# Performance work log

Measured on AMD Instinct MI355X. Metric: run time of the kernel, lower is better.

Reference implementation:

```python
import jax, jax.numpy as jnp
import numpy as np

B, L = 1, 320
CS, CZ, CH, H, PQ, PV = 384, 128, 16, 12, 4, 8
INF, EPS = 1e5, 1e-8


def _quat_to_rot(q):
    w, x, y, z = q[..., 0], q[..., 1], q[..., 2], q[..., 3]
    r0 = jnp.stack([1 - 2*(y*y + z*z), 2*(x*y - w*z), 2*(x*z + w*y)], -1)
    r1 = jnp.stack([2*(x*y + w*z), 1 - 2*(x*x + z*z), 2*(y*z - w*x)], -1)
    r2 = jnp.stack([2*(x*z - w*y), 2*(y*z + w*x), 1 - 2*(x*x + y*y)], -1)
    return jnp.stack([r0, r1, r2], -2)


def setup_inputs():
    key = jax.random.key(0)
    ks = jax.random.split(key, 12)

    def lin(k, fan_in, fan_out):
        k1, k2 = jax.random.split(k)
        lim = 1.0 / np.sqrt(fan_in)
        return (jax.random.uniform(k1, (fan_in, fan_out), minval=-lim, maxval=lim, dtype=jnp.float32),
                jax.random.uniform(k2, (fan_out,), minval=-lim, maxval=lim, dtype=jnp.float32))

    s = jax.random.normal(ks[0], (B, L, CS), dtype=jnp.float32)
    quat = jax.random.normal(ks[1], (B, L, 4), dtype=jnp.float32)
    quat = quat / jnp.linalg.norm(quat, axis=-1, keepdims=True)
    rot = _quat_to_rot(quat)                                   # proper rotations (B,L,3,3)
    trans = 10.0 * jax.random.normal(ks[2], (B, L, 3), dtype=jnp.float32)
    z = jax.random.normal(ks[3], (B, L, L, CZ), dtype=jnp.float32)
    frame_mask = jnp.ones((B, L), dtype=jnp.float32)

    Wq, bq = lin(ks[4], CS, CH * H)
    Wkv, bkv = lin(ks[5], CS, 2 * CH * H)
    Wqp, bqp = lin(ks[6], CS, 6 * H * PQ)
    Wkvp, bkvp = lin(ks[7], CS, 6 * H * (PQ + PV))
    Wg, bg = lin(ks[8], CS, H * PQ)
    geom_weights = jnp.ones((3,), jnp.float32)
    dir_weight = jnp.asarray(0.5, jnp.float32)
    head_weights = 0.02 * jax.random.normal(ks[9], (H,), dtype=jnp.float32)
    concat_dim = H * (CH + 7 * PV) + H * CZ                    # 2400
    Wo, bo = lin(ks[10], concat_dim, CS)
    return dict(s=s, rot=rot, trans=trans, z=z, frame_mask=frame_mask,
                Wq=Wq, bq=bq, Wkv=Wkv, bkv=bkv, Wqp=Wqp, bqp=bqp,
                Wkvp=Wkvp, bkvp=bkvp, Wg=Wg, bg=bg,
                geom_weights=geom_weights, dir_weight=dir_weight,
                head_weights=head_weights, Wo=Wo, bo=bo)


def reference(s, rot, trans, z, frame_mask, Wq, bq, Wkv, bkv, Wqp, bqp,
              Wkvp, bkvp, Wg, bg, geom_weights, dir_weight, head_weights, Wo, bo):
    def proc_pts(pts_flat, P):
        # (B,L,6*H*P) -> rotate coords+translate, rotate dirs -> (B,L,H,P,6)
        pts = pts_flat.reshape(B, L, H, P, 6)
        coords = jnp.einsum('blij,blhpj->blhpi', rot, pts[..., :3]) + trans[:, :, None, None, :]
        dirs = jnp.einsum('blij,blhpj->blhpi', rot, pts[..., 3:])
        return jnp.concatenate([coords, dirs], -1)

    q = (s @ Wq + bq).reshape(B, L, H, CH)
    kv = s @ Wkv + bkv
    k = kv[..., :CH * H].reshape(B, L, H, CH)
    v = kv[..., CH * H:].reshape(B, L, H, CH)

    q_pts = proc_pts(s @ Wqp + bqp, PQ)
    kv_pts = s @ Wkvp + bkvp
    k_pts = proc_pts(kv_pts[..., :6 * H * PQ], PQ)
    v_pts = proc_pts(kv_pts[..., 6 * H * PQ:], PV)

    gate = jax.nn.sigmoid(s @ Wg + bg).reshape(B, L, H, PQ, 1)
    q_pts = q_pts * gate

    scalar_att = jnp.einsum('bqhc,bkhc->bhqk', q, k) / np.sqrt(CH).astype(np.float32)

    # position attention: per-pair point distances + log + inverse, mean over points
    delta = q_pts[:, :, None, :, :, :3] - k_pts[:, None, :, :, :, :3]   # (B,Lq,Lk,H,PQ,3)
    d = jnp.linalg.norm(delta, axis=-1)
    pos_att = (d + jnp.log(d + EPS) + 1.0 / (d + EPS)).mean(-1).transpose(0, 3, 1, 2)

    # direction attention: per-point dot minus cross-product 'curvature'
    qd, kd = q_pts[..., 3:], k_pts[..., 3:]
    dot = jnp.einsum('bqhpd,bkhpd->bqkhp', qd, kd)                       # (B,Lq,Lk,H,P)
    cr = jnp.cross(qd[:, :, None, :, None, :, :], kd[:, None, :, :, :, None, :])  # (B,Lq,Lk,H,Pk,Pq,3)
    cross = jnp.linalg.norm(cr, axis=-1).mean(-1)                        # (B,Lq,Lk,H,Pk)
    nq = jnp.linalg.norm(qd, axis=-1)[:, :, None]                        # (B,Lq,1,H,P)
    nk = jnp.linalg.norm(kd, axis=-1)[:, None]                           # (B,1,Lk,H,P)
    dir_att = (dot - cross / (nq * nk + EPS)).mean(-1).transpose(0, 3, 1, 2)

    att = scalar_att + dir_weight * (geom_weights[0] * pos_att + geom_weights[1] * dir_att)
    att = att * head_weights[:, None, None]
    mask2d = frame_mask[:, None, None, :] * frame_mask[:, None, :, None]  # (B,1,L,L)
    att = jax.nn.softmax(att + INF * (mask2d - 1.0), axis=-1)

    o_scalar = jnp.einsum('bhqk,bkhc->bqhc', att, v)
    o_geom = jnp.einsum('bhqk,bkhpd->bqhpd', att, v_pts)                 # (B,L,H,PV,6)

    # map aggregated geometry back into local frames
    rotT = jnp.swapaxes(rot, -1, -2)
    trans_inv = -jnp.einsum('blij,blj->bli', rotT, trans)
    lc = jnp.einsum('blij,blhpj->blhpi', rotT, o_geom[..., :3]) + trans_inv[:, :, None, None, :]
    ld = jnp.einsum('blij,blhpj->blhpi', rotT, o_geom[..., 3:6])
    ld = ld / jnp.maximum(jnp.linalg.norm(ld, axis=-1, keepdims=True), 1e-12)  # F.normalize
    ln = jnp.linalg.norm(lc, axis=-1, keepdims=True)
    o_geom7 = jnp.concatenate([lc, ld, ln], -1)                          # (B,L,H,PV,7)

    o_pair = jnp.einsum('bhij,bijk->bihk', att, z)                       # (B,L,H,CZ)
    out = jnp.concatenate([o_scalar.reshape(B, L, H * CH),
                           o_geom7.reshape(B, L, H * PV * 7),
                           o_pair.reshape(B, L, H * CZ)], -1)
    return out @ Wo + bo
```

## Files before the change

### kernel.cpp

```cpp
#include <hip/hip_runtime.h>
#include <hip/hip_bf16.h>
#include <math.h>

#define LSEQ 320
#define CS 384
#define CZ 128
#define CH 16
#define NH 12
#define PQ 4
#define PV 8
#define EPSF 1e-8f

typedef short short8 __attribute__((ext_vector_type(8)));
typedef float f32x4 __attribute__((ext_vector_type(4)));
typedef unsigned short ush2 __attribute__((ext_vector_type(2)));

__device__ __forceinline__ unsigned short f2b(float x) {
    union { float f; unsigned u; } v; v.f = x;
    unsigned r = (v.u + 0x7FFF + ((v.u >> 16) & 1)) >> 16;
    return (unsigned short)r;
}
__device__ __forceinline__ float b2f(unsigned short h) {
    union { unsigned u; float f; } v; v.u = ((unsigned)h) << 16;
    return v.f;
}

#define OFF_Q       0
#define OFF_KV      61440
#define OFF_QPT     184320
#define OFF_SHI     276480
#define OFF_SMID    337920
#define OFF_SLO     399360
#define OFF_ATTHI   552960
#define OFF_PARTG   552960
#define OFF_CCHI    2191360
#define OFF_BCAT    4074496
#define OFF_VKVHI   4997872
#define OFF_VKVLO   5120752
#define OFF_QPR     5243632
#define OFF_KVPR    5335792
#define OFF_GATE    5612272
#define OFF_KROW    6242032
#define OFF_WCTHI   6426352
#define OFF_WCTMID  6767344
#define OFF_WCTLO   7108336
#define OFF_WOTHI   7449328
#define OFF_WOTLO   7910128

__global__ __launch_bounds__(256) void k_cast(
    const float* __restrict__ s,
    const float* __restrict__ bq, const float* __restrict__ bkv,
    const float* __restrict__ bqp, const float* __restrict__ bkvp,
    const float* __restrict__ bg,
    unsigned short* __restrict__ s_hi, unsigned short* __restrict__ s_mid,
    unsigned short* __restrict__ s_lo,
    float* __restrict__ bcat)
{
    int i = blockIdx.x * 256 + threadIdx.x;
    if (i < 122880) {
        float x = s[i];
        unsigned short hi = f2b(x);
        float r1 = x - b2f(hi);
        unsigned short mid = f2b(r1);
        s_hi[i] = hi; s_mid[i] = mid; s_lo[i] = f2b(r1 - b2f(mid));
        return;
    }
    i -= 122880;
    if (i < 1776) {
        float v;
        if (i < 192)       v = bq[i];
        else if (i < 576)  v = bkv[i - 192];
        else if (i < 864)  v = bqp[i - 576];
        else if (i < 1728) v = bkvp[i - 864];
        else               v = bg[i - 1728];
        bcat[i] = v;
    }
}

__global__ __launch_bounds__(256) void k_wtr(
    const float* __restrict__ Wq, const float* __restrict__ Wkv,
    const float* __restrict__ Wqp, const float* __restrict__ Wkvp,
    const float* __restrict__ Wg, const float* __restrict__ Wo,
    unsigned short* __restrict__ wcT_hi, unsigned short* __restrict__ wcT_mid,
    unsigned short* __restrict__ wcT_lo,
    unsigned short* __restrict__ woT_hi, unsigned short* __restrict__ woT_lo)
{
    __shared__ unsigned short th[64][65], tm[64][65], tl[64][65];
    int bid = blockIdx.x, tid = threadIdx.x;
    if (bid < 168) {
        int k0 = (bid % 6) * 64, c0 = (bid / 6) * 64;
        #pragma unroll
        for (int rep = 0; rep < 16; rep++) {
            int idx = rep * 256 + tid;
            int i = idx >> 6, j = idx & 63;
            int c = c0 + j, k = k0 + i;
            float v = 0.f;
            if (c < 1776) {
                if (c < 192)       v = Wq[(size_t)k * 192 + c];
                else if (c < 576)  v = Wkv[(size_t)k * 384 + c - 192];
                else if (c < 864)  v = Wqp[(size_t)k * 288 + c - 576];
                else if (c < 1728) v = Wkvp[(size_t)k * 864 + c - 864];
                else               v = Wg[(size_t)k * 48 + c - 1728];
            }
            unsigned short hi = f2b(v);
            float r1 = v - b2f(hi);
            unsigned short mid = f2b(r1);
            th[i][j] = hi; tm[i][j] = mid; tl[i][j] = f2b(r1 - b2f(mid));
        }
        __syncthreads();
        #pragma unroll
        for (int rep = 0; rep < 16; rep++) {
            int idx = rep * 256 + tid;
            int i = idx >> 6, j = idx & 63;
            int c = c0 + i;
            if (c < 1776) {
                size_t o = (size_t)c * 384 + k0 + j;
                wcT_hi[o] = th[j][i]; wcT_mid[o] = tm[j][i]; wcT_lo[o] = tl[j][i];
            }
        }
    } else {
        int b = bid - 168;
        int r0 = (b % 38) * 64, c0 = (b / 38) * 64;
        #pragma unroll
        for (int rep = 0; rep < 16; rep++) {
            int idx = rep * 256 + tid;
            int i = idx >> 6, j = idx & 63;
            int r = r0 + i;
            float v = 0.f;
            if (r < 2400) v = Wo[(size_t)r * 384 + c0 + j];
            unsigned short hi = f2b(v);
            th[i][j] = hi; tl[i][j] = f2b(v - b2f(hi));
        }
        __syncthreads();
        #pragma unroll
        for (int rep = 0; rep < 16; rep++) {
            int idx = rep * 256 + tid;
            int i = idx >> 6, j = idx & 63;
            int r = r0 + j;
            if (r < 2400) {
                size_t o = (size_t)(c0 + i) * 2400 + r;
                woT_hi[o] = th[j][i]; woT_lo[o] = tl[j][i];
            }
        }
    }
}

__global__ __launch_bounds__(192) void k_proj(
    const unsigned short* __restrict__ s_hi, const unsigned short* __restrict__ s_mid,
    const unsigned short* __restrict__ s_lo,
    const unsigned short* __restrict__ wcT_hi, const unsigned short* __restrict__ wcT_mid,
    const unsigned short* __restrict__ wcT_lo,
    const float* __restrict__ bcat,
    float* __restrict__ qo, float* __restrict__ kvo,
    float* __restrict__ qpr, float* __restrict__ kvpr, float* __restrict__ gate)
{
    __shared__ unsigned short a_h[16][56], a_m[16][56], a_l[16][56];
    __shared__ unsigned short w_h[48][56], w_m[48][56], w_l[48][56];
    int col0 = blockIdx.x * 48, l0 = blockIdx.y * 16;
    int tid = threadIdx.x;
    int lane = tid & 63, w = tid >> 6;
    int ncol = lane & 15, blk = lane >> 4, mrow = (lane >> 4) * 4;

    float* dst; int nc, cbase; bool sig = false;
    if (col0 < 192)       { nc = 192; cbase = col0;        dst = qo;   }
    else if (col0 < 576)  { nc = 384; cbase = col0 - 192;  dst = kvo;  }
    else if (col0 < 864)  { nc = 288; cbase = col0 - 576;  dst = qpr;  }
    else if (col0 < 1728) { nc = 864; cbase = col0 - 864;  dst = kvpr; }
    else                  { nc = 48;  cbase = 0;           dst = gate; sig = true; }

    f32x4 acc = {};
    for (int k0 = 0; k0 < 384; k0 += 32) {
        __syncthreads();
        {
            int arr = tid >> 6, idx = tid & 63;
            int row = idx >> 2, seg = idx & 3;
            size_t off = (size_t)(l0 + row) * 384 + k0 + seg * 8;
            if (arr == 0)      *(short8*)&a_h[row][seg * 8] = *(const short8*)(s_hi + off);
            else if (arr == 1) *(short8*)&a_m[row][seg * 8] = *(const short8*)(s_mid + off);
            else               *(short8*)&a_l[row][seg * 8] = *(const short8*)(s_lo + off);
        }
        {
            int row = tid >> 2, seg = tid & 3;
            size_t off = (size_t)(col0 + row) * 384 + k0 + seg * 8;
            *(short8*)&w_h[row][seg * 8] = *(const short8*)(wcT_hi + off);
            *(short8*)&w_m[row][seg * 8] = *(const short8*)(wcT_mid + off);
            *(short8*)&w_l[row][seg * 8] = *(const short8*)(wcT_lo + off);
        }
        __syncthreads();
        short8 afh = *(short8*)&a_h[ncol][blk * 8];
        short8 afm = *(short8*)&a_m[ncol][blk * 8];
        short8 afl = *(short8*)&a_l[ncol][blk * 8];
        short8 bfh = *(short8*)&w_h[w * 16 + ncol][blk * 8];
        short8 bfm = *(short8*)&w_m[w * 16 + ncol][blk * 8];
        short8 bfl = *(short8*)&w_l[w * 16 + ncol][blk * 8];
        acc = __builtin_amdgcn_mfma_f32_16x16x32_bf16(afm, bfm, acc, 0, 0, 0);
        acc = __builtin_amdgcn_mfma_f32_16x16x32_bf16(afh, bfl, acc, 0, 0, 0);
        acc = __builtin_amdgcn_mfma_f32_16x16x32_bf16(afl, bfh, acc, 0, 0, 0);
        acc = __builtin_amdgcn_mfma_f32_16x16x32_bf16(afh, bfm, acc, 0, 0, 0);
        acc = __builtin_amdgcn_mfma_f32_16x16x32_bf16(afm, bfh, acc, 0, 0, 0);
        acc = __builtin_amdgcn_mfma_f32_16x16x32_bf16(afh, bfh, acc, 0, 0, 0);
    }
    {
        int n = w * 16 + ncol;
        float bv = bcat[col0 + n];
        int cloc = cbase + n;
        #pragma unroll
        for (int r = 0; r < 4; r++) {
            float v2 = acc[r] + bv;
            if (sig) v2 = 1.0f / (1.0f + expf(-v2));
            dst[(size_t)(l0 + mrow + r) * nc + cloc] = v2;
        }
    }
}

__global__ __launch_bounds__(256) void k_points(
    const float* __restrict__ qpr, const float* __restrict__ kvpr, const float* __restrict__ gate,
    const float* __restrict__ rot, const float* __restrict__ trans,
    const float* __restrict__ kv,
    float* __restrict__ qpt, float* __restrict__ krow,
    unsigned short* __restrict__ vkv_hi, unsigned short* __restrict__ vkv_lo)
{
    __shared__ float vsh[96][6];
    __shared__ float kp_s[48][6];
    __shared__ float kn_s[48];
    int l = blockIdx.x, t = threadIdx.x;
    const float* R = rot + l * 9;
    float tx = trans[l * 3], ty = trans[l * 3 + 1], tz = trans[l * 3 + 2];
    if (t < 192) {
        const float* src; float g = 1.0f; float* dst = nullptr; int vj = -1, kj = -1;
        if (t < 48)      { src = qpr + (size_t)l * 288 + t * 6; g = gate[l * 48 + t]; dst = qpt + ((size_t)l * 48 + t) * 6; }
        else if (t < 96) { kj = t - 48; src = kvpr + (size_t)l * 864 + kj * 6; }
        else             { int j = t - 96; src = kvpr + (size_t)l * 864 + 288 + j * 6; vj = j; }
        float px = src[0], py = src[1], pz = src[2], ux = src[3], uy = src[4], uz = src[5];
        float c0 = R[0] * px + R[1] * py + R[2] * pz + tx;
        float c1 = R[3] * px + R[4] * py + R[5] * pz + ty;
        float c2 = R[6] * px + R[7] * py + R[8] * pz + tz;
        float d0 = R[0] * ux + R[1] * uy + R[2] * uz;
        float d1 = R[3] * ux + R[4] * uy + R[5] * uz;
        float d2 = R[6] * ux + R[7] * uy + R[8] * uz;
        if (vj >= 0) {
            vsh[vj][0] = c0; vsh[vj][1] = c1; vsh[vj][2] = c2;
            vsh[vj][3] = d0; vsh[vj][4] = d1; vsh[vj][5] = d2;
        } else if (kj >= 0) {
            kp_s[kj][0] = c0; kp_s[kj][1] = c1; kp_s[kj][2] = c2;
            kp_s[kj][3] = d0; kp_s[kj][4] = d1; kp_s[kj][5] = d2;
            kn_s[kj] = sqrtf(d0 * d0 + d1 * d1 + d2 * d2);
        } else {
            dst[0] = c0 * g; dst[1] = c1 * g; dst[2] = c2 * g;
            dst[3] = d0 * g; dst[4] = d1 * g; dst[5] = d2 * g;
        }
    }
    __syncthreads();
    #pragma unroll
    for (int e = 0; e < 3; e++) {
        int u = t * 3 + e;
        int h = u >> 6, n = u & 63;
        float val;
        if (n < 16) val = kv[(size_t)l * 384 + 192 + h * 16 + n];
        else        val = vsh[h * 8 + (n - 16) / 6][(n - 16) % 6];
        unsigned short hi = f2b(val);
        size_t idx = ((size_t)h * 64 + n) * 320 + l;
        vkv_hi[idx] = hi;
        vkv_lo[idx] = f2b(val - b2f(hi));
    }
    for (int idx = t; idx < 576; idx += 256) {
        int h = idx / 48, j = idx - h * 48;
        float v;
        if (j < 24)      v = kp_s[h * 4 + j / 6][j % 6];
        else if (j < 40) v = kv[(size_t)l * 384 + h * 16 + (j - 24)];
        else if (j < 44) v = kn_s[h * 4 + (j - 40)];
        else             v = 0.0f;
        krow[((size_t)h * 320 + l) * 48 + j] = v;
    }
}

__global__ __launch_bounds__(256) void k_att(
    const float* __restrict__ qb, const float* __restrict__ qpt,
    const float* __restrict__ krow,
    const float* __restrict__ fm, const float* __restrict__ gw,
    const float* __restrict__ dwp, const float* __restrict__ hwp,
    float* __restrict__ att)
{
    int tid = threadIdx.x;
    int w = tid >> 6, lane = tid & 63;
    int iqA = blockIdx.x * 8 + w * 2;
    int iqB = iqA + 1;
    int h = blockIdx.y;

    float qvA[CH], qvB[CH];
    #pragma unroll
    for (int c = 0; c < CH; c++) {
        qvA[c] = qb[(size_t)iqA * 192 + h * CH + c];
        qvB[c] = qb[(size_t)iqB * 192 + h * CH + c];
    }
    float qpA[24], qpB[24];
    #pragma unroll
    for (int j = 0; j < 24; j++) {
        qpA[j] = qpt[(size_t)iqA * 288 + h * 24 + j];
        qpB[j] = qpt[(size_t)iqB * 288 + h * 24 + j];
    }
    float nqA[PQ], nq2A[PQ], nqB[PQ], nq2B[PQ];
    #pragma unroll
    for (int p = 0; p < PQ; p++) {
        float x = qpA[p * 6 + 3], y = qpA[p * 6 + 4], zz = qpA[p * 6 + 5];
        nq2A[p] = x * x + y * y + zz * zz; nqA[p] = sqrtf(nq2A[p]);
        x = qpB[p * 6 + 3]; y = qpB[p * 6 + 4]; zz = qpB[p * 6 + 5];
        nq2B[p] = x * x + y * y + zz * zz; nqB[p] = sqrtf(nq2B[p]);
    }
    float dwv = dwp[0], g0 = gw[0], g1 = gw[1], hwv = hwp[h];
    float fmA = fm[iqA], fmB = fm[iqB];

    float lgA[5], lgB[5];
    for (int r = 0; r < 5; r++) {
        int kk = r * 64 + lane;
        const float* rowp = krow + ((size_t)h * 320 + kk) * 48;
        float rw[44];
        #pragma unroll
        for (int j = 0; j < 44; j++) rw[j] = rowp[j];
        float fmk = fm[kk];

        #pragma unroll
        for (int which = 0; which < 2; which++) {
            const float* qp = which ? qpB : qpA;
            const float* qv = which ? qvB : qvA;
            const float* nq = which ? nqB : nqA;
            const float* nq2 = which ? nq2B : nq2A;
            float fmi = which ? fmB : fmA;

            float scalar = 0.f;
            #pragma unroll
            for (int c = 0; c < CH; c++) scalar += qv[c] * rw[24 + c];
            scalar *= 0.25f;

            float pos = 0.f;
            #pragma unroll
            for (int p = 0; p < PQ; p++) {
                float dx = qp[p * 6] - rw[p * 6];
                float dy = qp[p * 6 + 1] - rw[p * 6 + 1];
                float dz = qp[p * 6 + 2] - rw[p * 6 + 2];
                float d = __builtin_amdgcn_sqrtf(dx * dx + dy * dy + dz * dz);
                float de = d + EPSF;
                pos += d + __logf(de) + __builtin_amdgcn_rcpf(de);
            }
            pos *= 0.25f;

            float dir = 0.f;
            #pragma unroll
            for (int p = 0; p < PQ; p++) {
                float kx = rw[p * 6 + 3], ky = rw[p * 6 + 4], kz = rw[p * 6 + 5];
                float nk = rw[40 + p];
                float nk2 = nk * nk;
                float cm = 0.f, dself = 0.f;
                #pragma unroll
                for (int pq = 0; pq < PQ; pq++) {
                    float dq = qp[pq * 6 + 3] * kx + qp[pq * 6 + 4] * ky + qp[pq * 6 + 5] * kz;
                    if (pq == p) dself = dq;
                    cm += __builtin_amdgcn_sqrtf(fmaxf(nq2[pq] * nk2 - dq * dq, 0.0f));
                }
                cm *= 0.25f;
                dir += dself - cm * __builtin_amdgcn_rcpf(nq[p] * nk + EPSF);
            }
            dir *= 0.25f;

            float logit = scalar + dwv * (g0 * pos + g1 * dir);
            logit *= hwv;
            logit += 100000.0f * (fmi * fmk - 1.0f);
            if (which) lgB[r] = logit; else lgA[r] = logit;
        }
    }

    float mxA = lgA[0];
    #pragma unroll
    for (int r = 1; r < 5; r++) mxA = fmaxf(mxA, lgA[r]);
    for (int m = 32; m; m >>= 1) mxA = fmaxf(mxA, __shfl_xor(mxA, m, 64));
    float eA[5], smA = 0.f;
    #pragma unroll
    for (int r = 0; r < 5; r++) { eA[r] = __expf(lgA[r] - mxA); smA += eA[r]; }
    for (int m = 32; m; m >>= 1) smA += __shfl_xor(smA, m, 64);
    float invA = 1.0f / smA;
    #pragma unroll
    for (int r = 0; r < 5; r++)
        att[((size_t)h * 320 + iqA) * 320 + r * 64 + lane] = eA[r] * invA;
    float mxB = lgB[0];
    #pragma unroll
    for (int r = 1; r < 5; r++) mxB = fmaxf(mxB, lgB[r]);
    for (int m = 32; m; m >>= 1) mxB = fmaxf(mxB, __shfl_xor(mxB, m, 64));
    float eB[5], smB = 0.f;
    #pragma unroll
    for (int r = 0; r < 5; r++) { eB[r] = __expf(lgB[r] - mxB); smB += eB[r]; }
    for (int m = 32; m; m >>= 1) smB += __shfl_xor(smB, m, 64);
    float invB = 1.0f / smB;
    #pragma unroll
    for (int r = 0; r < 5; r++)
        att[((size_t)h * 320 + iqB) * 320 + r * 64 + lane] = eB[r] * invB;
}

__global__ __launch_bounds__(256) void k_sv(
    const float* __restrict__ att,
    const unsigned short* __restrict__ vkv_hi, const unsigned short* __restrict__ vkv_lo,
    const float* __restrict__ rot, const float* __restrict__ trans,
    float* __restrict__ cc)
{
    __shared__ unsigned short a_hi[16][56];
    __shared__ unsigned short a_lo[16][56];
    __shared__ unsigned short B[128][56];
    __shared__ float ogsh[16][49];
    int bid = blockIdx.x;
    int iq0 = (bid % 20) * 16, h = bid / 20;
    int tid = threadIdx.x;
    int lane = tid & 63, w = tid >> 6;
    int ncol = lane & 15, blk = lane >> 4, mrow = (lane >> 4) * 4;

    f32x4 acc = {};
    for (int k0 = 0; k0 < 320; k0 += 32) {
        __syncthreads();
        {
            int row = tid >> 4, c2 = (tid & 15) * 2;
            const float* ap = att + ((size_t)h * 320 + iq0 + row) * 320 + k0 + c2;
            float v0 = ap[0], v1 = ap[1];
            ush2 h2, l2;
            h2[0] = f2b(v0); l2[0] = f2b(v0 - b2f(h2[0]));
            h2[1] = f2b(v1); l2[1] = f2b(v1 - b2f(h2[1]));
            *(ush2*)&a_hi[row][c2] = h2;
            *(ush2*)&a_lo[row][c2] = l2;
        }
        {
            int row = tid >> 2, seg = tid & 3;
            size_t off = ((size_t)h * 64 + row) * 320 + k0 + seg * 8;
            *(short8*)&B[row][seg * 8]      = *(const short8*)(vkv_hi + off);
            *(short8*)&B[64 + row][seg * 8] = *(const short8*)(vkv_lo + off);
        }
        __syncthreads();
        short8 afh = *(short8*)&a_hi[ncol][blk * 8];
        short8 afl = *(short8*)&a_lo[ncol][blk * 8];
        short8 bfh = *(short8*)&B[w * 16 + ncol][blk * 8];
        short8 bfl = *(short8*)&B[64 + w * 16 + ncol][blk * 8];
        acc = __builtin_amdgcn_mfma_f32_16x16x32_bf16(afh, bfh, acc, 0, 0, 0);
        acc = __builtin_amdgcn_mfma_f32_16x16x32_bf16(afh, bfl, acc, 0, 0, 0);
        acc = __builtin_amdgcn_mfma_f32_16x16x32_bf16(afl, bfh, acc, 0, 0, 0);
    }
    {
        int n = w * 16 + ncol;
        #pragma unroll
        for (int r = 0; r < 4; r++) {
            int iq = iq0 + mrow + r;
            float v = acc[r];
            if (n < 16) cc[(size_t)iq * 2400 + h * 16 + n] = v;
            else        ogsh[mrow + r][n - 16] = v;
        }
    }
    __syncthreads();
    if (tid < 128) {
        int iqr = tid >> 3, p = tid & 7;
        int l = iq0 + iqr;
        const float* R = rot + l * 9;
        float tx = trans[l * 3], ty = trans[l * 3 + 1], tz = trans[l * 3 + 2];
        const float* o = &ogsh[iqr][p * 6];
        float gx = o[0] - tx, gy = o[1] - ty, gz = o[2] - tz;
        float l0 = R[0] * gx + R[3] * gy + R[6] * gz;
        float l1 = R[1] * gx + R[4] * gy + R[7] * gz;
        float l2 = R[2] * gx + R[5] * gy + R[8] * gz;
        float dx = o[3], dy = o[4], dz = o[5];
        float e0 = R[0] * dx + R[3] * dy + R[6] * dz;
        float e1 = R[1] * dx + R[4] * dy + R[7] * dz;
        float e2 = R[2] * dx + R[5] * dy + R[8] * dz;
        float n = sqrtf(e0 * e0 + e1 * e1 + e2 * e2);
        float inv = 1.0f / fmaxf(n, 1e-12f);
        float ln = sqrtf(l0 * l0 + l1 * l1 + l2 * l2);
        float vals[7] = { l0, l1, l2, e0 * inv, e1 * inv, e2 * inv, ln };
        size_t base = (size_t)l * 2400 + 192 + (h * PV + p) * 7;
        #pragma unroll
        for (int j = 0; j < 7; j++) cc[base + j] = vals[j];
    }
}

__global__ __launch_bounds__(256) void k_pair(
    const float* __restrict__ att,
    const float* __restrict__ z,
    float* __restrict__ cc)
{
    __shared__ unsigned short a_hi[16][56];
    __shared__ unsigned short a_lo[16][56];
    __shared__ unsigned short B[128][56];
    int iq = blockIdx.x, tid = threadIdx.x;
    int lane = tid & 63, w = tid >> 6;
    int ncol = lane & 15, blk = lane >> 4, mrow = (lane >> 4) * 4;
    int kp2 = (tid & 15) * 2;
    int cb = (tid >> 4) * 8;
    const float* zbase = z + ((size_t)iq * 320 + kp2) * 128 + cb;

    float4 zA0, zA1, zA2, zA3, zB0, zB1, zB2, zB3;
    {
        const float* p = zbase;
        zA0 = *(const float4*)(p);       zA1 = *(const float4*)(p + 4);
        zA2 = *(const float4*)(p + 128); zA3 = *(const float4*)(p + 132);
        p = zbase + (size_t)32 * 128;
        zB0 = *(const float4*)(p);       zB1 = *(const float4*)(p + 4);
        zB2 = *(const float4*)(p + 128); zB3 = *(const float4*)(p + 132);
    }

    f32x4 acc[2] = {};
    #pragma unroll
    for (int i = 0; i < 10; i++) {
        int k0 = i * 32;
        __syncthreads();
        {
            int row = tid >> 4, c2 = (tid & 15) * 2;
            float v0 = 0.f, v1 = 0.f;
            if (row < 12) {
                const float* ap = att + ((size_t)row * 320 + iq) * 320 + k0 + c2;
                v0 = ap[0]; v1 = ap[1];
            }
            ush2 h2, l2;
            h2[0] = f2b(v0); l2[0] = f2b(v0 - b2f(h2[0]));
            h2[1] = f2b(v1); l2[1] = f2b(v1 - b2f(h2[1]));
            *(ush2*)&a_hi[row][c2] = h2;
            *(ush2*)&a_lo[row][c2] = l2;
        }
        {
            float va[8], vb[8];
            if ((i & 1) == 0) {
                va[0]=zA0.x; va[1]=zA0.y; va[2]=zA0.z; va[3]=zA0.w;
                va[4]=zA1.x; va[5]=zA1.y; va[6]=zA1.z; va[7]=zA1.w;
                vb[0]=zA2.x; vb[1]=zA2.y; vb[2]=zA2.z; vb[3]=zA2.w;
                vb[4]=zA3.x; vb[5]=zA3.y; vb[6]=zA3.z; vb[7]=zA3.w;
            } else {
                va[0]=zB0.x; va[1]=zB0.y; va[2]=zB0.z; va[3]=zB0.w;
                va[4]=zB1.x; va[5]=zB1.y; va[6]=zB1.z; va[7]=zB1.w;
                vb[0]=zB2.x; vb[1]=zB2.y; vb[2]=zB2.z; vb[3]=zB2.w;
                vb[4]=zB3.x; vb[5]=zB3.y; vb[6]=zB3.z; vb[7]=zB3.w;
            }
            #pragma unroll
            for (int c = 0; c < 8; c++) {
                ush2 pr;
                pr[0] = f2b(va[c]);
                pr[1] = f2b(vb[c]);
                *(ush2*)&B[cb + c][kp2] = pr;
            }
            if (i + 2 < 10) {
                const float* p = zbase + (size_t)(k0 + 64) * 128;
                if ((i & 1) == 0) {
                    zA0 = *(const float4*)(p);       zA1 = *(const float4*)(p + 4);
                    zA2 = *(const float4*)(p + 128); zA3 = *(const float4*)(p + 132);
                } else {
                    zB0 = *(const float4*)(p);       zB1 = *(const float4*)(p + 4);
                    zB2 = *(const float4*)(p + 128); zB3 = *(const float4*)(p + 132);
                }
            }
        }
        __syncthreads();
        short8 afh = *(short8*)&a_hi[ncol][blk * 8];
        short8 afl = *(short8*)&a_lo[ncol][blk * 8];
        #pragma unroll
        for (int s2 = 0; s2 < 2; s2++) {
            short8 bf = *(short8*)&B[w * 32 + s2 * 16 + ncol][blk * 8];
            acc[s2] = __builtin_amdgcn_mfma_f32_16x16x32_bf16(afl, bf, acc[s2], 0, 0, 0);
            acc[s2] = __builtin_amdgcn_mfma_f32_16x16x32_bf16(afh, bf, acc[s2], 0, 0, 0);
        }
    }
    #pragma unroll
    for (int s2 = 0; s2 < 2; s2++) {
        int n = w * 32 + s2 * 16 + ncol;
        #pragma unroll
        for (int r = 0; r < 4; r++) {
            int h = mrow + r;
            if (h < 12)
                cc[(size_t)iq * 2400 + 864 + (size_t)h * 128 + n] = acc[s2][r];
        }
    }
}

__global__ __launch_bounds__(256) void k_gemm(
    const float* __restrict__ cc,
    const unsigned short* __restrict__ woT_hi, const unsigned short* __restrict__ woT_lo,
    float* __restrict__ part)
{
    __shared__ unsigned short a_h[16][56], a_l[16][56];
    __shared__ unsigned short w_h[64][56], w_l[64][56];
    int iq0 = blockIdx.x * 16, col0 = blockIdx.y * 64, ks = blockIdx.z;
    int tid = threadIdx.x;
    int lane = tid & 63, w = tid >> 6;
    int ncol = lane & 15, blk = lane >> 4, mrow = (lane >> 4) * 4;

    f32x4 acc = {};
    for (int kc = 0; kc < 15; kc++) {
        int k0 = ks * 480 + kc * 32;
        __syncthreads();
        {
            int row = tid >> 4, c2 = (tid & 15) * 2;
            const float* ap = cc + (size_t)(iq0 + row) * 2400 + k0 + c2;
            float v0 = ap[0], v1 = ap[1];
            ush2 h2, l2;
            h2[0] = f2b(v0); l2[0] = f2b(v0 - b2f(h2[0]));
            h2[1] = f2b(v1); l2[1] = f2b(v1 - b2f(h2[1]));
            *(ush2*)&a_h[row][c2] = h2;
            *(ush2*)&a_l[row][c2] = l2;
        }
        #pragma unroll
        for (int t2 = 0; t2 < 2; t2++) {
            int idx = tid * 2 + t2;
            int arr = idx >> 8, i2 = idx & 255;
            int row = i2 >> 2, seg = i2 & 3;
            size_t off = (size_t)(col0 + row) * 2400 + k0 + seg * 8;
            if (arr == 0) *(short8*)&w_h[row][seg * 8] = *(const short8*)(woT_hi + off);
            else          *(short8*)&w_l[row][seg * 8] = *(const short8*)(woT_lo + off);
        }
        __syncthreads();
        short8 afh = *(short8*)&a_h[ncol][blk * 8];
        short8 afl = *(short8*)&a_l[ncol][blk * 8];
        short8 bfh = *(short8*)&w_h[w * 16 + ncol][blk * 8];
        short8 bfl = *(short8*)&w_l[w * 16 + ncol][blk * 8];
        acc = __builtin_amdgcn_mfma_f32_16x16x32_bf16(afh, bfh, acc, 0, 0, 0);
        acc = __builtin_amdgcn_mfma_f32_16x16x32_bf16(afh, bfl, acc, 0, 0, 0);
        acc = __builtin_amdgcn_mfma_f32_16x16x32_bf16(afl, bfh, acc, 0, 0, 0);
    }
    {
        int cn = col0 + w * 16 + ncol;
        #pragma unroll
        for (int r = 0; r < 4; r++)
            part[((size_t)ks * 320 + iq0 + mrow + r) * 384 + cn] = acc[r];
    }
}

__global__ __launch_bounds__(256) void k_reduce(
    const float* __restrict__ part, const float* __restrict__ bo, float* __restrict__ out)
{
    int i = blockIdx.x * 256 + threadIdx.x;
    float v = bo[i % CS];
    #pragma unroll
    for (int ks = 0; ks < 5; ks++) v += part[(size_t)ks * 122880 + i];
    out[i] = v;
}

extern "C" void kernel_launch(void* const* d_in, const int* in_sizes, int n_in,
                              void* d_out, int out_size, void* d_ws, size_t ws_size,
                              hipStream_t stream)
{
    const float* s     = (const float*)d_in[0];
    const float* rot   = (const float*)d_in[1];
    const float* trans = (const float*)d_in[2];
    const float* z     = (const float*)d_in[3];
    const float* fm    = (const float*)d_in[4];
    const float* Wq    = (const float*)d_in[5];
    const float* bq    = (const float*)d_in[6];
    const float* Wkv   = (const float*)d_in[7];
    const float* bkv   = (const float*)d_in[8];
    const float* Wqp   = (const float*)d_in[9];
    const float* bqp   = (const float*)d_in[10];
    const float* Wkvp  = (const float*)d_in[11];
    const float* bkvp  = (const float*)d_in[12];
    const float* Wg    = (const float*)d_in[13];
    const float* bg    = (const float*)d_in[14];
    const float* gw    = (const float*)d_in[15];
    const float* dw    = (const float*)d_in[16];
    const float* hw    = (const float*)d_in[17];
    const float* Wo    = (const float*)d_in[18];
    const float* bo    = (const float*)d_in[19];

    float* ws = (float*)d_ws;
    float*          q       = ws + OFF_Q;
    float*          kv      = ws + OFF_KV;
    float*          qpt     = ws + OFF_QPT;
    float*          att     = ws + OFF_ATTHI;
    float*          part    = ws + OFF_PARTG;
    float*          cc      = ws + OFF_CCHI;
    unsigned short* s_hi    = (unsigned short*)(ws + OFF_SHI);
    unsigned short* s_mid   = (unsigned short*)(ws + OFF_SMID);
    unsigned short* s_lo    = (unsigned short*)(ws + OFF_SLO);
    float*          bcat    = ws + OFF_BCAT;
    unsigned short* vkv_hi  = (unsigned short*)(ws + OFF_VKVHI);
    unsigned short* vkv_lo  = (unsigned short*)(ws + OFF_VKVLO);
    float*          qpr     = ws + OFF_QPR;
    float*          kvpr    = ws + OFF_KVPR;
    float*          gate    = ws + OFF_GATE;
    float*          krow    = ws + OFF_KROW;
    unsigned short* wcT_hi  = (unsigned short*)(ws + OFF_WCTHI);
    unsigned short* wcT_mid = (unsigned short*)(ws + OFF_WCTMID);
    unsigned short* wcT_lo  = (unsigned short*)(ws + OFF_WCTLO);
    unsigned short* woT_hi  = (unsigned short*)(ws + OFF_WOTHI);
    unsigned short* woT_lo  = (unsigned short*)(ws + OFF_WOTLO);
    float* out = (float*)d_out;

    k_cast<<<dim3(487), dim3(256), 0, stream>>>(s, bq, bkv, bqp, bkvp, bg,
                                                s_hi, s_mid, s_lo, bcat);
    k_wtr<<<dim3(396), dim3(256), 0, stream>>>(Wq, Wkv, Wqp, Wkvp, Wg, Wo,
                                               wcT_hi, wcT_mid, wcT_lo, woT_hi, woT_lo);
    k_proj<<<dim3(37, 20), dim3(192), 0, stream>>>(s_hi, s_mid, s_lo, wcT_hi, wcT_mid, wcT_lo,
                                                   bcat, q, kv, qpr, kvpr, gate);
    k_points<<<dim3(LSEQ), dim3(256), 0, stream>>>(qpr, kvpr, gate, rot, trans, kv,
                                                   qpt, krow, vkv_hi, vkv_lo);
    k_att<<<dim3(40, NH), dim3(256), 0, stream>>>(q, qpt, krow, fm, gw, dw, hw, att);
    k_sv<<<dim3(240), dim3(256), 0, stream>>>(att, vkv_hi, vkv_lo, rot, trans, cc);
    k_pair<<<dim3(LSEQ), dim3(256), 0, stream>>>(att, z, cc);
    k_gemm<<<dim3(20, 6, 5), dim3(256), 0, stream>>>(cc, woT_hi, woT_lo, part);
    k_reduce<<<dim3(480), dim3(256), 0, stream>>>(part, bo, out);
}
```

Measured before the change: 213.0 us.

## Merge prep kernels and sv/pair kernels; stage key rows in LDS for attention

Merges the cast and weight-transpose kernels into one launch, and the scalar/point value aggregation and pair aggregation kernels into one launch with block-index dispatch. This cuts launch count and lets independent blocks fill the GPU together. The attention kernel now loads the per-head key rows (320x45 floats) into shared memory once per block instead of reading them from global memory in each wave. The large shared array may reduce occupancy in k_att.

```diff
diff --git a/kernel.cpp b/kernel.cpp
--- a/kernel.cpp
+++ b/kernel.cpp
@@ -47,46 +47,45 @@
 #define OFF_WOTHI   7449328
 #define OFF_WOTLO   7910128
 
-__global__ __launch_bounds__(256) void k_cast(
+__global__ __launch_bounds__(256) void k_prep(
     const float* __restrict__ s,
-    const float* __restrict__ bq, const float* __restrict__ bkv,
-    const float* __restrict__ bqp, const float* __restrict__ bkvp,
-    const float* __restrict__ bg,
+    const float* __restrict__ Wq, const float* __restrict__ bq,
+    const float* __restrict__ Wkv, const float* __restrict__ bkv,
+    const float* __restrict__ Wqp, const float* __restrict__ bqp,
+    const float* __restrict__ Wkvp, const float* __restrict__ bkvp,
+    const float* __restrict__ Wg, const float* __restrict__ bg,
+    const float* __restrict__ Wo,
     unsigned short* __restrict__ s_hi, unsigned short* __restrict__ s_mid,
-    unsigned short* __restrict__ s_lo,
-    float* __restrict__ bcat)
-{
-    int i = blockIdx.x * 256 + threadIdx.x;
-    if (i < 122880) {
-        float x = s[i];
-        unsigned short hi = f2b(x);
-        float r1 = x - b2f(hi);
-        unsigned short mid = f2b(r1);
-        s_hi[i] = hi; s_mid[i] = mid; s_lo[i] = f2b(r1 - b2f(mid));
-        return;
-    }
-    i -= 122880;
-    if (i < 1776) {
-        float v;
-        if (i < 192)       v = bq[i];
-        else if (i < 576)  v = bkv[i - 192];
-        else if (i < 864)  v = bqp[i - 576];
-        else if (i < 1728) v = bkvp[i - 864];
-        else               v = bg[i - 1728];
-        bcat[i] = v;
-    }
-}
-
-__global__ __launch_bounds__(256) void k_wtr(
-    const float* __restrict__ Wq, const float* __restrict__ Wkv,
-    const float* __restrict__ Wqp, const float* __restrict__ Wkvp,
-    const float* __restrict__ Wg, const float* __restrict__ Wo,
+    unsigned short* __restrict__ s_lo, float* __restrict__ bcat,
     unsigned short* __restrict__ wcT_hi, unsigned short* __restrict__ wcT_mid,
     unsigned short* __restrict__ wcT_lo,
     unsigned short* __restrict__ woT_hi, unsigned short* __restrict__ woT_lo)
 {
     __shared__ unsigned short th[64][65], tm[64][65], tl[64][65];
     int bid = blockIdx.x, tid = threadIdx.x;
+    if (bid < 487) {
+        int i = bid * 256 + tid;
+        if (i < 122880) {
+            float x = s[i];
+            unsigned short hi = f2b(x);
+            float r1 = x - b2f(hi);
+            unsigned short mid = f2b(r1);
+            s_hi[i] = hi; s_mid[i] = mid; s_lo[i] = f2b(r1 - b2f(mid));
+            return;
+        }
+        i -= 122880;
+        if (i < 1776) {
+            float v;
+            if (i < 192)       v = bq[i];
+            else if (i < 576)  v = bkv[i - 192];
+            else if (i < 864)  v = bqp[i - 576];
+            else if (i < 1728) v = bkvp[i - 864];
+            else               v = bg[i - 1728];
+            bcat[i] = v;
+        }
+        return;
+    }
+    bid -= 487;
     if (bid < 168) {
         int k0 = (bid % 6) * 64, c0 = (bid / 6) * 64;
         #pragma unroll
@@ -281,12 +280,18 @@
     const float* __restrict__ dwp, const float* __restrict__ hwp,
     float* __restrict__ att)
 {
+    __shared__ float ksh[320][45];
     int tid = threadIdx.x;
     int w = tid >> 6, lane = tid & 63;
     int iqA = blockIdx.x * 8 + w * 2;
     int iqB = iqA + 1;
     int h = blockIdx.y;
 
+    for (int idx = tid; idx < 320 * 48; idx += 256) {
+        int kk = idx / 48, j = idx - kk * 48;
+        if (j < 45) ksh[kk][j] = krow[((size_t)h * 320 + kk) * 48 + j];
+    }
+
     float qvA[CH], qvB[CH];
     #pragma unroll
     for (int c = 0; c < CH; c++) {
@@ -309,11 +314,12 @@
     }
     float dwv = dwp[0], g0 = gw[0], g1 = gw[1], hwv = hwp[h];
     float fmA = fm[iqA], fmB = fm[iqB];
+    __syncthreads();
 
     float lgA[5], lgB[5];
     for (int r = 0; r < 5; r++) {
         int kk = r * 64 + lane;
-        const float* rowp = krow + ((size_t)h * 320 + kk) * 48;
+        const float* rowp = &ksh[kk][0];
         float rw[44];
         #pragma unroll
         for (int j = 0; j < 44; j++) rw[j] = rowp[j];
@@ -395,9 +401,10 @@
         att[((size_t)h * 320 + iqB) * 320 + r * 64 + lane] = eB[r] * invB;
 }
 
-__global__ __launch_bounds__(256) void k_sv(
+__global__ __launch_bounds__(256) void k_svpair(
     const float* __restrict__ att,
     const unsigned short* __restrict__ vkv_hi, const unsigned short* __restrict__ vkv_lo,
+    const float* __restrict__ z,
     const float* __restrict__ rot, const float* __restrict__ trans,
     float* __restrict__ cc)
 {
@@ -406,166 +413,157 @@
     __shared__ unsigned short B[128][56];
     __shared__ float ogsh[16][49];
     int bid = blockIdx.x;
-    int iq0 = (bid % 20) * 16, h = bid / 20;
     int tid = threadIdx.x;
     int lane = tid & 63, w = tid >> 6;
     int ncol = lane & 15, blk = lane >> 4, mrow = (lane >> 4) * 4;
 
-    f32x4 acc = {};
-    for (int k0 = 0; k0 < 320; k0 += 32) {
+    if (bid < 240) {
+        int iq0 = (bid % 20) * 16, h = bid / 20;
+        f32x4 acc = {};
+        for (int k0 = 0; k0 < 320; k0 += 32) {
+            __syncthreads();
+            {
+                int row = tid >> 4, c2 = (tid & 15) * 2;
+                const float* ap = att + ((size_t)h * 320 + iq0 + row) * 320 + k0 + c2;
+                float v0 = ap[0], v1 = ap[1];
+                ush2 h2, l2;
+                h2[0] = f2b(v0); l2[0] = f2b(v0 - b2f(h2[0]));
+                h2[1] = f2b(v1); l2[1] = f2b(v1 - b2f(h2[1]));
+                *(ush2*)&a_hi[row][c2] = h2;
+                *(ush2*)&a_lo[row][c2] = l2;
+            }
+            {
+                int row = tid >> 2, seg = tid & 3;
+                size_t off = ((size_t)h * 64 + row) * 320 + k0 + seg * 8;
+                *(short8*)&B[row][seg * 8]      = *(const short8*)(vkv_hi + off);
+                *(short8*)&B[64 + row][seg * 8] = *(const short8*)(vkv_lo + off);
+            }
+            __syncthreads();
+            short8 afh = *(short8*)&a_hi[ncol][blk * 8];
+            short8 afl = *(short8*)&a_lo[ncol][blk * 8];
+            short8 bfh = *(short8*)&B[w * 16 + ncol][blk * 8];
+            short8 bfl = *(short8*)&B[64 + w * 16 + ncol][blk * 8];
+            acc = __builtin_amdgcn_mfma_f32_16x16x32_bf16(afh, bfh, acc, 0, 0, 0);
+            acc = __builtin_amdgcn_mfma_f32_16x16x32_bf16(afh, bfl, acc, 0, 0, 0);
+            acc = __builtin_amdgcn_mfma_f32_16x16x32_bf16(afl, bfh, acc, 0, 0, 0);
+        }
+        {
+            int n = w * 16 + ncol;
+            #pragma unroll
+            for (int r = 0; r < 4; r++) {
+                int iq = iq0 + mrow + r;
+                float v = acc[r];
+                if (n < 16) cc[(size_t)iq * 2400 + h * 16 + n] = v;
+                else        ogsh[mrow + r][n - 16] = v;
+            }
+        }
         __syncthreads();
+        if (tid < 128) {
+            int iqr = tid >> 3, p = tid & 7;
+            int l = iq0 + iqr;
+            const float* R = rot + l * 9;
+            float tx = trans[l * 3], ty = trans[l * 3 + 1], tz = trans[l * 3 + 2];
+            const float* o = &ogsh[iqr][p * 6];
+            float gx = o[0] - tx, gy = o[1] - ty, gz = o[2] - tz;
+            float l0 = R[0] * gx + R[3] * gy + R[6] * gz;
+            float l1 = R[1] * gx + R[4] * gy + R[7] * gz;
+            float l2 = R[2] * gx + R[5] * gy + R[8] * gz;
+            float dx = o[3], dy = o[4], dz = o[5];
+            float e0 = R[0] * dx + R[3] * dy + R[6] * dz;
+            float e1 = R[1] * dx + R[4] * dy + R[7] * dz;
+            float e2 = R[2] * dx + R[5] * dy + R[8] * dz;
+            float n = sqrtf(e0 * e0 + e1 * e1 + e2 * e2);
+            float inv = 1.0f / fmaxf(n, 1e-12f);
+            float ln = sqrtf(l0 * l0 + l1 * l1 + l2 * l2);
+            float vals[7] = { l0, l1, l2, e0 * inv, e1 * inv, e2 * inv, ln };
+            size_t base = (size_t)l * 2400 + 192 + (h * PV + p) * 7;
+            #pragma unroll
+            for (int j = 0; j < 7; j++) cc[base + j] = vals[j];
+        }
+    } else {
+        int iq = bid - 240;
+        int kp2 = (tid & 15) * 2;
+        int cb = (tid >> 4) * 8;
+        const float* zbase = z + ((size_t)iq * 320 + kp2) * 128 + cb;
+
+        float4 zA0, zA1, zA2, zA3, zB0, zB1, zB2, zB3;
         {
-            int row = tid >> 4, c2 = (tid & 15) * 2;
-            const float* ap = att + ((size_t)h * 320 + iq0 + row) * 320 + k0 + c2;
-            float v0 = ap[0], v1 = ap[1];
-            ush2 h2, l2;
-            h2[0] = f2b(v0); l2[0] = f2b(v0 - b2f(h2[0]));
-            h2[1] = f2b(v1); l2[1] = f2b(v1 - b2f(h2[1]));
-            *(ush2*)&a_hi[row][c2] = h2;
-            *(ush2*)&a_lo[row][c2] = l2;
-        }
-        {
-            int row = tid >> 2, seg = tid & 3;
-            size_t off = ((size_t)h * 64 + row) * 320 + k0 + seg * 8;
-            *(short8*)&B[row][seg * 8]      = *(const short8*)(vkv_hi + off);
-            *(short8*)&B[64 + row][seg * 8] = *(const short8*)(vkv_lo + off);
-        }
-        __syncthreads();
-        short8 afh = *(short8*)&a_hi[ncol][blk * 8];
-        short8 afl = *(short8*)&a_lo[ncol][blk * 8];
-        short8 bfh = *(short8*)&B[w * 16 + ncol][blk * 8];
-        short8 bfl = *(short8*)&B[64 + w * 16 + ncol][blk * 8];
-        acc = __builtin_amdgcn_mfma_f32_16x16x32_bf16(afh, bfh, acc, 0, 0, 0);
-        acc = __builtin_amdgcn_mfma_f32_16x16x32_bf16(afh, bfl, acc, 0, 0, 0);
-        acc = __builtin_amdgcn_mfma_f32_16x16x32_bf16(afl, bfh, acc, 0, 0, 0);
-    }
-    {
-        int n = w * 16 + ncol;
-        #pragma unroll
-        for (int r = 0; r < 4; r++) {
-            int iq = iq0 + mrow + r;
-            float v = acc[r];
-            if (n < 16) cc[(size_t)iq * 2400 + h * 16 + n] = v;
-            else        ogsh[mrow + r][n - 16] = v;
-        }
-    }
-    __syncthreads();
-    if (tid < 128) {
-        int iqr = tid >> 3, p = tid & 7;
-        int l = iq0 + iqr;
-        const float* R = rot + l * 9;
-        float tx = trans[l * 3], ty = trans[l * 3 + 1], tz = trans[l * 3 + 2];
-        const float* o = &ogsh[iqr][p * 6];
-        float gx = o[0] - tx, gy = o[1] - ty, gz = o[2] - tz;
-        float l0 = R[0] * gx + R[3] * gy + R[6] * gz;
-        float l1 = R[1] * gx + R[4] * gy + R[7] * gz;
-        float l2 = R[2] * gx + R[5] * gy + R[8] * gz;
-        float dx = o[3], dy = o[4], dz = o[5];
-        float e0 = R[0] * dx + R[3] * dy + R[6] * dz;
-        float e1 = R[1] * dx + R[4] * dy + R[7] * dz;
-        float e2 = R[2] * dx + R[5] * dy + R[8] * dz;
-        float n = sqrtf(e0 * e0 + e1 * e1 + e2 * e2);
-        float inv = 1.0f / fmaxf(n, 1e-12f);
-        float ln = sqrtf(l0 * l0 + l1 * l1 + l2 * l2);
-        float vals[7] = { l0, l1, l2, e0 * inv, e1 * inv, e2 * inv, ln };
-        size_t base = (size_t)l * 2400 + 192 + (h * PV + p) * 7;
-        #pragma unroll
-        for (int j = 0; j < 7; j++) cc[base + j] = vals[j];
-    }
-}
-
-__global__ __launch_bounds__(256) void k_pair(
-    const float* __restrict__ att,
-    const float* __restrict__ z,
-    float* __restrict__ cc)
-{
-    __shared__ unsigned short a_hi[16][56];
-    __shared__ unsigned short a_lo[16][56];
-    __shared__ unsigned short B[128][56];
-    int iq = blockIdx.x, tid = threadIdx.x;
-    int lane = tid & 63, w = tid >> 6;
-    int ncol = lane & 15, blk = lane >> 4, mrow = (lane >> 4) * 4;
-    int kp2 = (tid & 15) * 2;
-    int cb = (tid >> 4) * 8;
-    const float* zbase = z + ((size_t)iq * 320 + kp2) * 128 + cb;
-
-    float4 zA0, zA1, zA2, zA3, zB0, zB1, zB2, zB3;
-    {
-        const float* p = zbase;
-        zA0 = *(const float4*)(p);       zA1 = *(const float4*)(p + 4);
-        zA2 = *(const float4*)(p + 128); zA3 = *(const float4*)(p + 132);
-        p = zbase + (size_t)32 * 128;
-        zB0 = *(const float4*)(p);       zB1 = *(const float4*)(p + 4);
-        zB2 = *(const float4*)(p + 128); zB3 = *(const float4*)(p + 132);
-    }
-
-    f32x4 acc[2] = {};
-    #pragma unroll
-    for (int i = 0; i < 10; i++) {
-        int k0 = i * 32;
-        __syncthreads();
-        {
-            int row = tid >> 4, c2 = (tid & 15) * 2;
-            float v0 = 0.f, v1 = 0.f;
-            if (row < 12) {
-                const float* ap = att + ((size_t)row * 320 + iq) * 320 + k0 + c2;
-                v0 = ap[0]; v1 = ap[1];
-            }
-            ush2 h2, l2;
-            h2[0] = f2b(v0); l2[0] = f2b(v0 - b2f(h2[0]));
-            h2[1] = f2b(v1); l2[1] = f2b(v1 - b2f(h2[1]));
-            *(ush2*)&a_hi[row][c2] = h2;
-            *(ush2*)&a_lo[row][c2] = l2;
-        }
-        {
-            float va[8], vb[8];
-            if ((i & 1) == 0) {
-                va[0]=zA0.x; va[1]=zA0.y; va[2]=zA0.z; va[3]=zA0.w;
-                va[4]=zA1.x; va[5]=zA1.y; va[6]=zA1.z; va[7]=zA1.w;
-                vb[0]=zA2.x; vb[1]=zA2.y; vb[2]=zA2.z; vb[3]=zA2.w;
-                vb[4]=zA3.x; vb[5]=zA3.y; vb[6]=zA3.z; vb[7]=zA3.w;
-            } else {
-                va[0]=zB0.x; va[1]=zB0.y; va[2]=zB0.z; va[3]=zB0.w;
-                va[4]=zB1.x; va[5]=zB1.y; va[6]=zB1.z; va[7]=zB1.w;
-                vb[0]=zB2.x; vb[1]=zB2.y; vb[2]=zB2.z; vb[3]=zB2.w;
-                vb[4]=zB3.x; vb[5]=zB3.y; vb[6]=zB3.z; vb[7]=zB3.w;
-            }
+            const float* p = zbase;
+            zA0 = *(const float4*)(p);       zA1 = *(const float4*)(p + 4);
+            zA2 = *(const float4*)(p + 128); zA3 = *(const float4*)(p + 132);
+            p = zbase + (size_t)32 * 128;
+            zB0 = *(const float4*)(p);       zB1 = *(const float4*)(p + 4);
+            zB2 = *(const float4*)(p + 128); zB3 = *(const float4*)(p + 132);
+        }
+
+        f32x4 acc[2] = {};
+        #pragma unroll
+        for (int i = 0; i < 10; i++) {
+            int k0 = i * 32;
+            __syncthreads();
+            {
+                int row = tid >> 4, c2 = (tid & 15) * 2;
+                float v0 = 0.f, v1 = 0.f;
+                if (row < 12) {
+                    const float* ap = att + ((size_t)row * 320 + iq) * 320 + k0 + c2;
+                    v0 = ap[0]; v1 = ap[1];
+                }
+                ush2 h2, l2;
+                h2[0] = f2b(v0); l2[0] = f2b(v0 - b2f(h2[0]));
+                h2[1] = f2b(v1); l2[1] = f2b(v1 - b2f(h2[1]));
+                *(ush2*)&a_hi[row][c2] = h2;
+                *(ush2*)&a_lo[row][c2] = l2;
+            }
+            {
+                float va[8], vb[8];
+                if ((i & 1) == 0) {
+                    va[0]=zA0.x; va[1]=zA0.y; va[2]=zA0.z; va[3]=zA0.w;
+                    va[4]=zA1.x; va[5]=zA1.y; va[6]=zA1.z; va[7]=zA1.w;
+                    vb[0]=zA2.x; vb[1]=zA2.y; vb[2]=zA2.z; vb[3]=zA2.w;
+                    vb[4]=zA3.x; vb[5]=zA3.y; vb[6]=zA3.z; vb[7]=zA3.w;
+                } else {
+                    va[0]=zB0.x; va[1]=zB0.y; va[2]=zB0.z; va[3]=zB0.w;
+                    va[4]=zB1.x; va[5]=zB1.y; va[6]=zB1.z; va[7]=zB1.w;
+                    vb[0]=zB2.x; vb[1]=zB2.y; vb[2]=zB2.z; vb[3]=zB2.w;
+                    vb[4]=zB3.x; vb[5]=zB3.y; vb[6]=zB3.z; vb[7]=zB3.w;
+                }
+                #pragma unroll
+                for (int c = 0; c < 8; c++) {
+                    ush2 pr;
+                    pr[0] = f2b(va[c]);
+                    pr[1] = f2b(vb[c]);
+                    *(ush2*)&B[cb + c][kp2] = pr;
+                }
+                if (i + 2 < 10) {
+                    const float* p = zbase + (size_t)(k0 + 64) * 128;
+                    if ((i & 1) == 0) {
+                        zA0 = *(const float4*)(p);       zA1 = *(const float4*)(p + 4);
+                        zA2 = *(const float4*)(p + 128); zA3 = *(const float4*)(p + 132);
+                    } else {
+                        zB0 = *(const float4*)(p);       zB1 = *(const float4*)(p + 4);
+                        zB2 = *(const float4*)(p + 128); zB3 = *(const float4*)(p + 132);
+                    }
+                }
+            }
+            __syncthreads();
+            short8 afh = *(short8*)&a_hi[ncol][blk * 8];
+            short8 afl = *(short8*)&a_lo[ncol][blk * 8];
             #pragma unroll
-            for (int c = 0; c < 8; c++) {
-                ush2 pr;
-                pr[0] = f2b(va[c]);
-                pr[1] = f2b(vb[c]);
-                *(ush2*)&B[cb + c][kp2] = pr;
-            }
-            if (i + 2 < 10) {
-                const float* p = zbase + (size_t)(k0 + 64) * 128;
-                if ((i & 1) == 0) {
-                    zA0 = *(const float4*)(p);       zA1 = *(const float4*)(p + 4);
-                    zA2 = *(const float4*)(p + 128); zA3 = *(const float4*)(p + 132);
-                } else {
-                    zB0 = *(const float4*)(p);       zB1 = *(const float4*)(p + 4);
-                    zB2 = *(const float4*)(p + 128); zB3 = *(const float4*)(p + 132);
-                }
-            }
-        }
-        __syncthreads();
-        short8 afh = *(short8*)&a_hi[ncol][blk * 8];
-        short8 afl = *(short8*)&a_lo[ncol][blk * 8];
+            for (int s2 = 0; s2 < 2; s2++) {
+                short8 bf = *(short8*)&B[w * 32 + s2 * 16 + ncol][blk * 8];
+                acc[s2] = __builtin_amdgcn_mfma_f32_16x16x32_bf16(afl, bf, acc[s2], 0, 0, 0);
+                acc[s2] = __builtin_amdgcn_mfma_f32_16x16x32_bf16(afh, bf, acc[s2], 0, 0, 0);
+            }
+        }
         #pragma unroll
         for (int s2 = 0; s2 < 2; s2++) {
-            short8 bf = *(short8*)&B[w * 32 + s2 * 16 + ncol][blk * 8];
-            acc[s2] = __builtin_amdgcn_mfma_f32_16x16x32_bf16(afl, bf, acc[s2], 0, 0, 0);
-            acc[s2] = __builtin_amdgcn_mfma_f32_16x16x32_bf16(afh, bf, acc[s2], 0, 0, 0);
-        }
-    }
-    #pragma unroll
-    for (int s2 = 0; s2 < 2; s2++) {
-        int n = w * 32 + s2 * 16 + ncol;
-        #pragma unroll
-        for (int r = 0; r < 4; r++) {
-            int h = mrow + r;
-            if (h < 12)
-                cc[(size_t)iq * 2400 + 864 + (size_t)h * 128 + n] = acc[s2][r];
+            int n = w * 32 + s2 * 16 + ncol;
+            #pragma unroll
+            for (int r = 0; r < 4; r++) {
+                int h = mrow + r;
+                if (h < 12)
+                    cc[(size_t)iq * 2400 + 864 + (size_t)h * 128 + n] = acc[s2][r];
+            }
         }
     }
 }
@@ -681,17 +679,16 @@
     unsigned short* woT_lo  = (unsigned short*)(ws + OFF_WOTLO);
     float* out = (float*)d_out;
 
-    k_cast<<<dim3(487), dim3(256), 0, stream>>>(s, bq, bkv, bqp, bkvp, bg,
-                                                s_hi, s_mid, s_lo, bcat);
-    k_wtr<<<dim3(396), dim3(256), 0, stream>>>(Wq, Wkv, Wqp, Wkvp, Wg, Wo,
-                                               wcT_hi, wcT_mid, wcT_lo, woT_hi, woT_lo);
+    k_prep<<<dim3(883), dim3(256), 0, stream>>>(s, Wq, bq, Wkv, bkv, Wqp, bqp,
+                                                Wkvp, bkvp, Wg, bg, Wo,
+                                                s_hi, s_mid, s_lo, bcat,
+                                                wcT_hi, wcT_mid, wcT_lo, woT_hi, woT_lo);
     k_proj<<<dim3(37, 20), dim3(192), 0, stream>>>(s_hi, s_mid, s_lo, wcT_hi, wcT_mid, wcT_lo,
                                                    bcat, q, kv, qpr, kvpr, gate);
     k_points<<<dim3(LSEQ), dim3(256), 0, stream>>>(qpr, kvpr, gate, rot, trans, kv,
                                                    qpt, krow, vkv_hi, vkv_lo);
     k_att<<<dim3(40, NH), dim3(256), 0, stream>>>(q, qpt, krow, fm, gw, dw, hw, att);
-    k_sv<<<dim3(240), dim3(256), 0, stream>>>(att, vkv_hi, vkv_lo, rot, trans, cc);
-    k_pair<<<dim3(LSEQ), dim3(256), 0, stream>>>(att, z, cc);
+    k_svpair<<<dim3(560), dim3(256), 0, stream>>>(att, vkv_hi, vkv_lo, z, rot, trans, cc);
     k_gemm<<<dim3(20, 6, 5), dim3(256), 0, stream>>>(cc, woT_hi, woT_lo, part);
     k_reduce<<<dim3(480), dim3(256), 0, stream>>>(part, bo, out);
 }
```

Result: slower. 226.0 us (+6.1%).
